# Optimization experiments

Hardware: AMD Instinct MI355X
Metric: run time of the kernel (lower is better)

## Reference

```python
import jax, jax.numpy as jnp
import numpy as np

RADIUS = 0.05  # screen-space splat radius (NDC units), from raster_settings


def setup_inputs() -> dict:
    key = jax.random.key(0)
    k1, k2, k3 = jax.random.split(key, 3)
    B, N, C, H = 1, 4096, 8, 128
    # camera-space points: z in [2,4], xy chosen so NDC projection (x/z) covers [-1,1]
    z = jax.random.uniform(k1, (B, N, 1), minval=2.0, maxval=4.0)
    xy = jax.random.uniform(k2, (B, N, 2), minval=-1.0, maxval=1.0) * z
    points = jnp.concatenate([xy, z], axis=-1)  # [B,N,3]
    features = jax.random.normal(k3, (B, N, C), dtype=jnp.float32)
    return {"points": points, "features": features, "image_size": H, "points_per_pixel": 8}


def reference(points, features, image_size, points_per_pixel):
    B, N, _ = points.shape
    H = W = image_size
    K = points_per_pixel
    C = features.shape[-1]
    r2 = RADIUS * RADIUS

    x, y, z = points[..., 0], points[..., 1], points[..., 2]
    # perspective projection to NDC (focal length 1)
    px = x / z  # [B,N]
    py = y / z

    # pixel centers in NDC [-1,1]
    xs = (jnp.arange(W, dtype=jnp.float32) + 0.5) / W * 2.0 - 1.0
    ys = (jnp.arange(H, dtype=jnp.float32) + 0.5) / H * 2.0 - 1.0
    gy, gx = jnp.meshgrid(ys, xs, indexing="ij")
    gx = gx.reshape(-1)  # [P], P = H*W
    gy = gy.reshape(-1)

    # squared screen-space distance pixel<->point: [B, P, N]
    dx = gx[None, :, None] - px[:, None, :]
    dy = gy[None, :, None] - py[:, None, :]
    dist2 = dx * dx + dy * dy

    hit = (dist2 < r2) & (z[:, None, :] > 0.0)
    NEG = jnp.float32(-1e30)
    # K nearest-in-depth points per pixel among hits (top_k of -z)
    keys = jnp.where(hit, -z[:, None, :], NEG)
    negz, idx = jax.lax.top_k(keys, K)  # [B,P,K]
    valid = negz > NEG * 0.5

    d2k = jnp.take_along_axis(dist2, idx, axis=2)           # [B,P,K]
    fk = jax.vmap(lambda f, i: f[i])(features, idx)          # [B,P,K,C]

    # AlphaCompositor: w = 1 - d2/r^2, front-to-back compositing
    alpha = jnp.where(valid, jnp.clip(1.0 - d2k / r2, 0.0, 1.0), 0.0)
    trans = jnp.cumprod(1.0 - alpha, axis=-1)
    T = jnp.concatenate([jnp.ones_like(alpha[..., :1]), trans[..., :-1]], axis=-1)
    w = alpha * T                                            # [B,P,K]

    out = jnp.einsum("bpk,bpkc->bpc", w, fk)
    return out.reshape(B, H, W, C)
```

## Files before the change

### kernel.cpp

```cpp
#include <hip/hip_runtime.h>
#include <math.h>

#define RADIUS 0.05f
#define NTHREADS 1024
#define NSLICE   16
#define SPCAP   256
#define HCAP    40
#define HSTR    41

__global__ __launch_bounds__(1024) void render_tiles(
    const float* __restrict__ points,
    const float* __restrict__ features,
    float* __restrict__ out,
    int N, int H, int W, int tiles_x)
{
    const float r2 = RADIUS * RADIUS;
    const float inv_r2 = 1.0f / r2;

    __shared__ float4 sp[SPCAP];
    __shared__ float  s_hz[64 * HSTR];
    __shared__ float  s_hd[64 * HSTR];
    __shared__ int    s_hi[64 * HSTR];
    __shared__ int    s_pcnt[64];
    __shared__ int    s_cnt;

    if (threadIdx.x == 0) s_cnt = 0;
    if (threadIdx.x < 64) s_pcnt[threadIdx.x] = 0;
    __syncthreads();

    const int tile = blockIdx.x;
    const int tx = tile % tiles_x;
    const int ty = tile / tiles_x;
    const int x0i = tx * 8, y0i = ty * 8;
    const float sx = 2.0f / (float)W, sy = 2.0f / (float)H;
    const float bx0 = ((float)x0i + 0.5f) * sx - 1.0f - RADIUS;
    const float bx1 = ((float)(x0i + 7) + 0.5f) * sx - 1.0f + RADIUS;
    const float by0 = ((float)y0i + 0.5f) * sy - 1.0f - RADIUS;
    const float by1 = ((float)(y0i + 7) + 0.5f) * sy - 1.0f + RADIUS;

    for (int i = threadIdx.x; i < N; i += NTHREADS) {
        float x = points[3 * i + 0];
        float y = points[3 * i + 1];
        float z = points[3 * i + 2];
        bool keep = (z > 0.0f) & (x >= bx0 * z) & (x <= bx1 * z)
                               & (y >= by0 * z) & (y <= by1 * z);
        if (keep) {
            float rz = __builtin_amdgcn_rcpf(z);
            int pos = atomicAdd(&s_cnt, 1);
            if (pos < SPCAP) sp[pos] = make_float4(x * rz, y * rz, z, __int_as_float(i));
        }
    }
    __syncthreads();
    const int cnt = min(s_cnt, SPCAP);

    const int pxl = threadIdx.x & 63;
    const int slice = threadIdx.x >> 6;
    const int ix = x0i + (pxl & 7);
    const int iy = y0i + (pxl >> 3);
    const float gx = ((float)ix + 0.5f) * sx - 1.0f;
    const float gy = ((float)iy + 0.5f) * sy - 1.0f;

    int c = slice;
    if (c < cnt) {
        float4 q = sp[c];
        while (true) {
            int cn = c + NSLICE;
            bool more = cn < cnt;
            float4 qn = sp[more ? cn : slice];
            float dx = gx - q.x;
            float dy = gy - q.y;
            float d2 = dx * dx + dy * dy;
            if (d2 < r2) {
                int pos = atomicAdd(&s_pcnt[pxl], 1);
                if (pos < HCAP) {
                    s_hz[pxl * HSTR + pos] = q.z;
                    s_hd[pxl * HSTR + pos] = d2;
                    s_hi[pxl * HSTR + pos] = __float_as_int(q.w);
                }
            }
            if (!more) break;
            q = qn; c = cn;
        }
    }
    __syncthreads();

    if (threadIdx.x < 64) {
        const int m = min(s_pcnt[pxl], HCAP);
        float zk[8];
        int sk[8];
#pragma unroll
        for (int k = 0; k < 8; k++) { zk[k] = 3.0e38f; sk[k] = 0; }

        float z_next = s_hz[pxl * HSTR];
        for (int i = 0; i < m; i++) {
            float z = z_next;
            z_next = s_hz[pxl * HSTR + i + 1];
            if (z < zk[7]) {
                int s = i;
#pragma unroll
                for (int k = 0; k < 8; k++) {
                    bool lt = z < zk[k];
                    float tz = zk[k];
                    int ts = sk[k];
                    if (lt) { zk[k] = z; sk[k] = s; z = tz; s = ts; }
                }
            }
        }

        float acc0 = 0.f, acc1 = 0.f, acc2 = 0.f, acc3 = 0.f;
        float acc4 = 0.f, acc5 = 0.f, acc6 = 0.f, acc7 = 0.f;
        float T = 1.0f;
#pragma unroll
        for (int k = 0; k < 8; k++) {
            if (zk[k] < 1.0e30f) {
                float d2 = s_hd[pxl * HSTR + sk[k]];
                int   id = s_hi[pxl * HSTR + sk[k]];
                float alpha = 1.0f - d2 * inv_r2;
                alpha = fminf(fmaxf(alpha, 0.0f), 1.0f);
                float w = alpha * T;
                T *= (1.0f - alpha);
                const float4* f = (const float4*)(features + (size_t)id * 8);
                float4 f0 = f[0];
                float4 f1 = f[1];
                acc0 += w * f0.x; acc1 += w * f0.y; acc2 += w * f0.z; acc3 += w * f0.w;
                acc4 += w * f1.x; acc5 += w * f1.y; acc6 += w * f1.z; acc7 += w * f1.w;
            }
        }

        if (ix < W && iy < H) {
            float4* o = (float4*)(out + (size_t)(iy * W + ix) * 8);
            o[0] = make_float4(acc0, acc1, acc2, acc3);
            o[1] = make_float4(acc4, acc5, acc6, acc7);
        }
    }
}

extern "C" void kernel_launch(void* const* d_in, const int* in_sizes, int n_in,
                              void* d_out, int out_size, void* d_ws, size_t ws_size,
                              hipStream_t stream) {
    const float* points = (const float*)d_in[0];
    const float* features = (const float*)d_in[1];
    float* out = (float*)d_out;

    int N = in_sizes[0] / 3;
    int C = in_sizes[1] / N;
    int P = out_size / C;
    int H = (int)(sqrt((double)P) + 0.5);
    int W = H;
    int tiles_x = (W + 7) / 8;
    int tiles_y = (H + 7) / 8;

    render_tiles<<<tiles_x * tiles_y, NTHREADS, 0, stream>>>(points, features, out,
                                                             N, H, W, tiles_x);
}
```

Before: 70.52 us.

## Shrink tiles to 4x4 with 256-thread blocks, vectorize point loads, spread selection across waves

Tiles shrink from 8x8 to 4x4 pixels and blocks from 1024 to 256 threads, giving 1024 blocks instead of 256 so more CUs are busy and fewer points pass the per-tile cull. Point culling reads positions as float4 groups of four points, replacing scalar strided loads. The per-pixel top-8 selection and compositing now use 4 lanes in each of the 4 waves rather than one wave of 64 threads. In exchange, every block still scans all N points, so total global culling traffic across the grid grows about fourfold.

```diff
diff --git a/kernel.cpp b/kernel.cpp
--- a/kernel.cpp
+++ b/kernel.cpp
@@ -2,13 +2,15 @@
 #include <math.h>
 
 #define RADIUS 0.05f
-#define NTHREADS 1024
+#define NTHREADS 256
+#define TSZ      4
+#define NPIX     16
 #define NSLICE   16
-#define SPCAP   256
+#define SPCAP   192
 #define HCAP    40
 #define HSTR    41
 
-__global__ __launch_bounds__(1024) void render_tiles(
+__global__ __launch_bounds__(NTHREADS) void render_tiles(
     const float* __restrict__ points,
     const float* __restrict__ features,
     float* __restrict__ out,
@@ -18,27 +20,51 @@
     const float inv_r2 = 1.0f / r2;
 
     __shared__ float4 sp[SPCAP];
-    __shared__ float  s_hz[64 * HSTR];
-    __shared__ float  s_hd[64 * HSTR];
-    __shared__ int    s_hi[64 * HSTR];
-    __shared__ int    s_pcnt[64];
+    __shared__ float  s_hz[NPIX * HSTR];
+    __shared__ float  s_hd[NPIX * HSTR];
+    __shared__ int    s_hi[NPIX * HSTR];
+    __shared__ int    s_pcnt[NPIX];
     __shared__ int    s_cnt;
 
-    if (threadIdx.x == 0) s_cnt = 0;
-    if (threadIdx.x < 64) s_pcnt[threadIdx.x] = 0;
+    const int tid = threadIdx.x;
+    if (tid == 0) s_cnt = 0;
+    if (tid < NPIX) s_pcnt[tid] = 0;
     __syncthreads();
 
     const int tile = blockIdx.x;
     const int tx = tile % tiles_x;
     const int ty = tile / tiles_x;
-    const int x0i = tx * 8, y0i = ty * 8;
+    const int x0i = tx * TSZ, y0i = ty * TSZ;
     const float sx = 2.0f / (float)W, sy = 2.0f / (float)H;
     const float bx0 = ((float)x0i + 0.5f) * sx - 1.0f - RADIUS;
-    const float bx1 = ((float)(x0i + 7) + 0.5f) * sx - 1.0f + RADIUS;
+    const float bx1 = ((float)(x0i + TSZ - 1) + 0.5f) * sx - 1.0f + RADIUS;
     const float by0 = ((float)y0i + 0.5f) * sy - 1.0f - RADIUS;
-    const float by1 = ((float)(y0i + 7) + 0.5f) * sy - 1.0f + RADIUS;
+    const float by1 = ((float)(y0i + TSZ - 1) + 0.5f) * sy - 1.0f + RADIUS;
 
-    for (int i = threadIdx.x; i < N; i += NTHREADS) {
+    const float4* p4 = (const float4*)points;
+    const int N4 = N & ~3;
+    for (int i0 = tid * 4; i0 < N4; i0 += NTHREADS * 4) {
+        const int q = 3 * (i0 >> 2);
+        float4 a = p4[q + 0];
+        float4 b = p4[q + 1];
+        float4 c = p4[q + 2];
+        const float xs_[4] = {a.x, a.w, b.z, c.y};
+        const float ys_[4] = {a.y, b.x, b.w, c.z};
+        const float zs_[4] = {a.z, b.y, c.x, c.w};
+#pragma unroll
+        for (int j = 0; j < 4; j++) {
+            float x = xs_[j], y = ys_[j], z = zs_[j];
+            bool keep = (z > 0.0f) & (x >= bx0 * z) & (x <= bx1 * z)
+                                   & (y >= by0 * z) & (y <= by1 * z);
+            if (keep) {
+                float rz = __builtin_amdgcn_rcpf(z);
+                int pos = atomicAdd(&s_cnt, 1);
+                if (pos < SPCAP)
+                    sp[pos] = make_float4(x * rz, y * rz, z, __int_as_float(i0 + j));
+            }
+        }
+    }
+    for (int i = N4 + tid; i < N; i += NTHREADS) {
         float x = points[3 * i + 0];
         float y = points[3 * i + 1];
         float z = points[3 * i + 2];
@@ -53,10 +79,10 @@
     __syncthreads();
     const int cnt = min(s_cnt, SPCAP);
 
-    const int pxl = threadIdx.x & 63;
-    const int slice = threadIdx.x >> 6;
-    const int ix = x0i + (pxl & 7);
-    const int iy = y0i + (pxl >> 3);
+    const int pxl = tid & 15;
+    const int slice = tid >> 4;
+    const int ix = x0i + (pxl & 3);
+    const int iy = y0i + (pxl >> 2);
     const float gx = ((float)ix + 0.5f) * sx - 1.0f;
     const float gy = ((float)iy + 0.5f) * sy - 1.0f;
 
@@ -84,17 +110,20 @@
     }
     __syncthreads();
 
-    if (threadIdx.x < 64) {
-        const int m = min(s_pcnt[pxl], HCAP);
+    const int lane = tid & 63;
+    const int wave = tid >> 6;
+    if (lane < 4) {
+        const int p = wave * 4 + lane;
+        const int m = min(s_pcnt[p], HCAP);
         float zk[8];
         int sk[8];
 #pragma unroll
         for (int k = 0; k < 8; k++) { zk[k] = 3.0e38f; sk[k] = 0; }
 
-        float z_next = s_hz[pxl * HSTR];
+        float z_next = s_hz[p * HSTR];
         for (int i = 0; i < m; i++) {
             float z = z_next;
-            z_next = s_hz[pxl * HSTR + i + 1];
+            z_next = s_hz[p * HSTR + i + 1];
             if (z < zk[7]) {
                 int s = i;
 #pragma unroll
@@ -113,8 +142,8 @@
 #pragma unroll
         for (int k = 0; k < 8; k++) {
             if (zk[k] < 1.0e30f) {
-                float d2 = s_hd[pxl * HSTR + sk[k]];
-                int   id = s_hi[pxl * HSTR + sk[k]];
+                float d2 = s_hd[p * HSTR + sk[k]];
+                int   id = s_hi[p * HSTR + sk[k]];
                 float alpha = 1.0f - d2 * inv_r2;
                 alpha = fminf(fmaxf(alpha, 0.0f), 1.0f);
                 float w = alpha * T;
@@ -127,8 +156,10 @@
             }
         }
 
-        if (ix < W && iy < H) {
-            float4* o = (float4*)(out + (size_t)(iy * W + ix) * 8);
+        const int oix = x0i + (p & 3);
+        const int oiy = y0i + (p >> 2);
+        if (oix < W && oiy < H) {
+            float4* o = (float4*)(out + (size_t)(oiy * W + oix) * 8);
             o[0] = make_float4(acc0, acc1, acc2, acc3);
             o[1] = make_float4(acc4, acc5, acc6, acc7);
         }
@@ -147,8 +178,8 @@
     int P = out_size / C;
     int H = (int)(sqrt((double)P) + 0.5);
     int W = H;
-    int tiles_x = (W + 7) / 8;
-    int tiles_y = (H + 7) / 8;
+    int tiles_x = (W + TSZ - 1) / TSZ;
+    int tiles_y = (H + TSZ - 1) / TSZ;
 
     render_tiles<<<tiles_x * tiles_y, NTHREADS, 0, stream>>>(points, features, out,
                                                              N, H, W, tiles_x);
```

Result: slower. 75.27 us (+6.7%).
